# Kernel tuning notes

Measured on AMD Instinct MI355X. Metric: run time of the kernel, lower is better.

The kernel has to match this reference:

```python
import jax, jax.numpy as jnp
import numpy as np

N = 524288   # tokens (accounts)
D = 9        # num_prop_size
E = 2        # expert_size
H = 128      # expert MLP hidden
M = 32       # moe_out
O = 2        # output_size
K = 1        # top-k
LOSS_COF = 0.01
EPS = 1e-10


def setup_inputs() -> dict:
    key = jax.random.key(0)
    ks = jax.random.split(key, 10)
    f32 = jnp.float32
    return {
        "num_prop": jax.random.normal(ks[0], (N, D), f32),
        "cat_prop": jax.random.normal(ks[1], (N, 3), f32),
        "w_gate": jax.random.normal(ks[2], (D, E), f32) * 0.1,
        "W1": jax.random.normal(ks[3], (E, D, H), f32) * 0.1,
        "b1": jax.random.normal(ks[4], (E, H), f32) * 0.01,
        "W2": jax.random.normal(ks[5], (E, H, M), f32) * 0.1,
        "b2": jax.random.normal(ks[6], (E, M), f32) * 0.01,
        "Wout": jax.random.normal(ks[7], (M, O), f32) * 0.1,
        "bout": jax.random.normal(ks[8], (O,), f32) * 0.01,
        "k": K,
    }


def _cv_squared(x):
    # torch: x.var() (unbiased) / (x.mean()**2 + eps)
    return jnp.var(x, ddof=1) / (jnp.mean(x) ** 2 + EPS)


def reference(num_prop, cat_prop, w_gate, W1, b1, W2, b2, Wout, bout, k):
    x = num_prop                                   # eval mode: dropout = identity
    n, e = x.shape[0], w_gate.shape[1]

    # --- top-k gating (eval: clean logits, no noise) ---
    logits = x @ w_gate                            # [N, E]
    top_logits, top_idx = jax.lax.top_k(logits, min(k + 1, e))
    top_k_gates = jax.nn.softmax(top_logits[:, :k], axis=1)   # [N, k]
    rows = jnp.arange(n)[:, None]
    gates = jnp.zeros_like(logits).at[rows, top_idx[:, :k]].set(top_k_gates)  # [N, E]

    importance = gates.sum(axis=0)                 # [E]
    load = (gates > 0).astype(jnp.float32).sum(axis=0)  # [E]
    loss = (_cv_squared(importance) + _cv_squared(load)) * LOSS_COF

    # --- experts: per-expert 2-layer MLP, computed dense (E=2) then gated combine ---
    h = jax.nn.relu(jnp.einsum("nd,edh->neh", x, W1) + b1)    # [N, E, H]
    y_e = jnp.einsum("neh,ehm->nem", h, W2) + b2              # [N, E, M]
    y = jnp.einsum("ne,nem->nm", gates, y_e)                  # [N, M]

    out = y @ Wout + bout                                     # [N, O]
    return (out, loss)
```

## Files before the change

### kernel.cpp

```cpp
#include <hip/hip_runtime.h>
#include <hip/hip_bf16.h>

#define NTOK 524288
#define TPB  256
#define NBLK (NTOK / TPB)

__device__ __forceinline__ float bf2f(unsigned short u) {
    union { unsigned int i; float f; } v;
    v.i = ((unsigned int)u) << 16;
    return v.f;
}

__device__ __forceinline__ float ldq(const void* p, int i, bool f32) {
    if (f32) return ((const float*)p)[i];
    return bf2f(((const unsigned short*)p)[i]);
}

__global__ void prep_kernel(const void* __restrict__ num_prop,
                            const void* __restrict__ wgate,
                            const void* __restrict__ W1,
                            const void* __restrict__ b1,
                            const void* __restrict__ W2,
                            const void* __restrict__ b2,
                            const void* __restrict__ Wout,
                            const void* __restrict__ bout,
                            unsigned int* __restrict__ cnt1,
                            int* __restrict__ flag,
                            float* __restrict__ bpp,
                            float* __restrict__ wgf,
                            float* __restrict__ wpack)
{
    __shared__ int sflag;
    const int t = threadIdx.x;
    if (t == 0) {
        const unsigned short* u = (const unsigned short*)num_prop;
        int f = 0;
        for (int i = 0; i < 72; ++i) {
            int e = (u[i] >> 7) & 0xFF;
            if (e < 64 || e > 191) f = 1;
        }
        sflag = f; *flag = f; *cnt1 = 0u;
    }
    __syncthreads();
    const bool f32 = (sflag != 0);

    if (t < 18) wgf[t] = ldq(wgate, t, f32);

    if (t < 4) {
        int e = t >> 1, o = t & 1;
        float acc = ldq(bout, o, f32);
        for (int m = 0; m < 32; ++m)
            acc += ldq(b2, e * 32 + m, f32) * ldq(Wout, m * 2 + o, f32);
        bpp[t] = acc;
    }

    const int e = t >> 7;
    const int j = t & 127;
    float p0 = 0.f, p1 = 0.f;
    for (int m = 0; m < 32; ++m) {
        float w = ldq(W2, (e * 128 + j) * 32 + m, f32);
        p0 += w * ldq(Wout, m * 2 + 0, f32);
        p1 += w * ldq(Wout, m * 2 + 1, f32);
    }
    float* dst = wpack + j * 24 + e * 12;
    #pragma unroll
    for (int d = 0; d < 9; ++d)
        dst[d] = ldq(W1, (e * 9 + d) * 128 + j, f32);
    dst[9]  = ldq(b1, e * 128 + j, f32);
    dst[10] = p0;
    dst[11] = p1;
}

__global__ __launch_bounds__(TPB, 8)
void moe_main(const void* __restrict__ xg,
              const int* __restrict__ flag,
              const float* __restrict__ wgf,
              const float* __restrict__ bpp,
              const float* __restrict__ wpack,
              unsigned int* __restrict__ cnt1,
              float2* __restrict__ out)
{
    __shared__ float xs[TPB * 9];
    __shared__ unsigned int cblk;
    const int tid = threadIdx.x;
    if (tid == 0) cblk = 0u;

    const bool f32 = (*flag) != 0;
    const int base = blockIdx.x * (TPB * 9);
    if (f32) {
        const float* xf = (const float*)xg;
        for (int i = tid; i < TPB * 9; i += TPB)
            xs[i] = xf[base + i];
    } else {
        const unsigned short* xu = (const unsigned short*)xg;
        for (int i = tid; i < TPB * 9; i += TPB)
            xs[i] = bf2f(xu[base + i]);
    }
    __syncthreads();

    float x[9];
    #pragma unroll
    for (int d = 0; d < 9; ++d) x[d] = xs[tid * 9 + d];

    float l0 = 0.f, l1 = 0.f;
    #pragma unroll
    for (int d = 0; d < 9; ++d) {
        l0 = fmaf(x[d], wgf[d * 2 + 0], l0);
        l1 = fmaf(x[d], wgf[d * 2 + 1], l1);
    }
    const bool e1 = l1 > l0;

    unsigned long long bal = __ballot(e1);
    if ((tid & 63) == 0)
        atomicAdd(&cblk, (unsigned int)__popcll(bal));

    float a00 = bpp[0], a01 = bpp[1], a10 = bpp[2], a11 = bpp[3];

    #pragma unroll 4
    for (int j = 0; j < 128; ++j) {
        const float* wp = wpack + j * 24;
        float h0 = wp[9], h1 = wp[21];
        #pragma unroll
        for (int d = 0; d < 9; ++d) {
            h0 = fmaf(x[d], wp[d],      h0);
            h1 = fmaf(x[d], wp[12 + d], h1);
        }
        h0 = fmaxf(h0, 0.f);
        h1 = fmaxf(h1, 0.f);
        a00 = fmaf(h0, wp[10], a00);
        a01 = fmaf(h0, wp[11], a01);
        a10 = fmaf(h1, wp[22], a10);
        a11 = fmaf(h1, wp[23], a11);
    }

    float2 o;
    o.x = e1 ? a10 : a00;
    o.y = e1 ? a11 : a01;
    out[blockIdx.x * TPB + tid] = o;

    __syncthreads();
    if (tid == 0) atomicAdd(cnt1, cblk);
}

__global__ void finalize_kernel(const unsigned int* __restrict__ cnt1,
                                float* __restrict__ loss_out)
{
    double c1 = (double)(*cnt1);
    double c0 = (double)NTOK - c1;
    double diff = c0 - c1;
    double mean = (double)NTOK * 0.5;
    double var  = 0.5 * diff * diff;
    double cv2  = var / (mean * mean + 1e-10);
    *loss_out = (float)(0.02 * cv2);
}

extern "C" void kernel_launch(void* const* d_in, const int* in_sizes, int n_in,
                              void* d_out, int out_size, void* d_ws, size_t ws_size,
                              hipStream_t stream) {
    const void* num_prop = d_in[0];
    const void* w_gate   = d_in[2];
    const void* W1       = d_in[3];
    const void* b1       = d_in[4];
    const void* W2       = d_in[5];
    const void* b2       = d_in[6];
    const void* Wout     = d_in[7];
    const void* bout     = d_in[8];

    char* ws = (char*)d_ws;
    unsigned int* cnt1 = (unsigned int*)ws;
    int* flag          = (int*)(ws + 8);
    float* bpp         = (float*)(ws + 16);
    float* wgf         = (float*)(ws + 64);
    float* wpack       = (float*)(ws + 192);

    float*  outf = (float*)d_out;
    float2* out2 = (float2*)d_out;

    hipLaunchKernelGGL(prep_kernel, dim3(1), dim3(256), 0, stream,
                       num_prop, w_gate, W1, b1, W2, b2, Wout, bout,
                       cnt1, flag, bpp, wgf, wpack);
    hipLaunchKernelGGL(moe_main, dim3(NBLK), dim3(TPB), 0, stream,
                       num_prop, flag, wgf, bpp, wpack, cnt1, out2);
    hipLaunchKernelGGL(finalize_kernel, dim3(1), dim3(1), 0, stream,
                       cnt1, outf + (size_t)NTOK * 2);
}
```

Baseline: 145.8 us.

## Fuse loss finalize into main kernel and load inputs directly to registers

Removes the separate finalize kernel by having the last block, detected with an atomic ticket counter, compute the load-balancing loss. Replaces the LDS staging of token features with direct per-thread strided global loads into registers. Parallelizes the dtype-detection scan in the prep kernel across threads and lowers the launch-bounds occupancy hint from 8 to 6. This saves one kernel launch and the LDS round trip, at the cost of uncoalesced 9-element strided loads and a fence plus extra atomic per block.

```diff
diff --git a/kernel.cpp b/kernel.cpp
--- a/kernel.cpp
+++ b/kernel.cpp
@@ -25,24 +25,24 @@
                             const void* __restrict__ Wout,
                             const void* __restrict__ bout,
                             unsigned int* __restrict__ cnt1,
+                            unsigned int* __restrict__ done,
                             int* __restrict__ flag,
                             float* __restrict__ bpp,
                             float* __restrict__ wgf,
                             float* __restrict__ wpack)
 {
-    __shared__ int sflag;
+    __shared__ int sbad;
     const int t = threadIdx.x;
-    if (t == 0) {
-        const unsigned short* u = (const unsigned short*)num_prop;
-        int f = 0;
-        for (int i = 0; i < 72; ++i) {
-            int e = (u[i] >> 7) & 0xFF;
-            if (e < 64 || e > 191) f = 1;
-        }
-        sflag = f; *flag = f; *cnt1 = 0u;
+    if (t == 0) { sbad = 0; *cnt1 = 0u; *done = 0u; }
+    __syncthreads();
+    if (t < 72) {
+        unsigned short u = ((const unsigned short*)num_prop)[t];
+        int e = (u >> 7) & 0xFF;
+        if (e < 64 || e > 191) sbad = 1;
     }
     __syncthreads();
-    const bool f32 = (sflag != 0);
+    const bool f32 = (sbad != 0);
+    if (t == 0) *flag = sbad;
 
     if (t < 18) wgf[t] = ldq(wgate, t, f32);
 
@@ -71,36 +71,34 @@
     dst[11] = p1;
 }
 
-__global__ __launch_bounds__(TPB, 8)
+__global__ __launch_bounds__(TPB, 6)
 void moe_main(const void* __restrict__ xg,
               const int* __restrict__ flag,
               const float* __restrict__ wgf,
               const float* __restrict__ bpp,
               const float* __restrict__ wpack,
               unsigned int* __restrict__ cnt1,
-              float2* __restrict__ out)
+              unsigned int* __restrict__ done,
+              float2* __restrict__ out,
+              float* __restrict__ loss_out)
 {
-    __shared__ float xs[TPB * 9];
     __shared__ unsigned int cblk;
     const int tid = threadIdx.x;
     if (tid == 0) cblk = 0u;
+    __syncthreads();
 
     const bool f32 = (*flag) != 0;
-    const int base = blockIdx.x * (TPB * 9);
+    const int base = blockIdx.x * (TPB * 9) + tid * 9;
+    float x[9];
     if (f32) {
-        const float* xf = (const float*)xg;
-        for (int i = tid; i < TPB * 9; i += TPB)
-            xs[i] = xf[base + i];
+        const float* xf = (const float*)xg + base;
+        #pragma unroll
+        for (int d = 0; d < 9; ++d) x[d] = xf[d];
     } else {
-        const unsigned short* xu = (const unsigned short*)xg;
-        for (int i = tid; i < TPB * 9; i += TPB)
-            xs[i] = bf2f(xu[base + i]);
+        const unsigned short* xu = (const unsigned short*)xg + base;
+        #pragma unroll
+        for (int d = 0; d < 9; ++d) x[d] = bf2f(xu[d]);
     }
-    __syncthreads();
-
-    float x[9];
-    #pragma unroll
-    for (int d = 0; d < 9; ++d) x[d] = xs[tid * 9 + d];
 
     float l0 = 0.f, l1 = 0.f;
     #pragma unroll
@@ -139,19 +137,19 @@
     out[blockIdx.x * TPB + tid] = o;
 
     __syncthreads();
-    if (tid == 0) atomicAdd(cnt1, cblk);
-}
-
-__global__ void finalize_kernel(const unsigned int* __restrict__ cnt1,
-                                float* __restrict__ loss_out)
-{
-    double c1 = (double)(*cnt1);
-    double c0 = (double)NTOK - c1;
-    double diff = c0 - c1;
-    double mean = (double)NTOK * 0.5;
-    double var  = 0.5 * diff * diff;
-    double cv2  = var / (mean * mean + 1e-10);
-    *loss_out = (float)(0.02 * cv2);
+    if (tid == 0) {
+        atomicAdd(cnt1, cblk);
+        __threadfence();
+        unsigned int ticket = atomicAdd(done, 1u);
+        if (ticket == (unsigned int)(NBLK - 1)) {
+            double c1 = (double)atomicAdd(cnt1, 0u);
+            double c0 = (double)NTOK - c1;
+            double diff = c0 - c1;
+            double mean = (double)NTOK * 0.5;
+            double cv2  = (0.5 * diff * diff) / (mean * mean + 1e-10);
+            *loss_out = (float)(0.02 * cv2);
+        }
+    }
 }
 
 extern "C" void kernel_launch(void* const* d_in, const int* in_sizes, int n_in,
@@ -168,8 +166,9 @@
 
     char* ws = (char*)d_ws;
     unsigned int* cnt1 = (unsigned int*)ws;
+    unsigned int* done = (unsigned int*)(ws + 4);
     int* flag          = (int*)(ws + 8);
-    float* bpp         = (float*)(ws + 16);
+    float* bpp         = (float*)(ws + 32);
     float* wgf         = (float*)(ws + 64);
     float* wpack       = (float*)(ws + 192);
 
@@ -178,9 +177,8 @@
 
     hipLaunchKernelGGL(prep_kernel, dim3(1), dim3(256), 0, stream,
                        num_prop, w_gate, W1, b1, W2, b2, Wout, bout,
-                       cnt1, flag, bpp, wgf, wpack);
+                       cnt1, done, flag, bpp, wgf, wpack);
     hipLaunchKernelGGL(moe_main, dim3(NBLK), dim3(TPB), 0, stream,
-                       num_prop, flag, wgf, bpp, wpack, cnt1, out2);
-    hipLaunchKernelGGL(finalize_kernel, dim3(1), dim3(1), 0, stream,
-                       cnt1, outf + (size_t)NTOK * 2);
+                       num_prop, flag, wgf, bpp, wpack, cnt1, done,
+                       out2, outf + (size_t)NTOK * 2);
 }
```

Measured after the change: 169.6 us. 16.3% more time.
